# Optimization experiments

Measured on AMD Instinct MI355X. Metric: run time of the kernel, lower is better.

## Reference

```python
import jax, jax.numpy as jnp
import numpy as np

HIDDEN = 2048
NUM_HEADS = 16
HEAD_DIM = 128
INNER = NUM_HEADS * HEAD_DIM
ROPE_BASE = 10000.0


def apply_rope(x):
    # x: [B, H, S, D], rotate-half (NeoX-style) RoPE
    B, H, S, D = x.shape
    inv_freq = 1.0 / (ROPE_BASE ** (jnp.arange(0, D, 2, dtype=jnp.float32) / D))
    t = jnp.arange(S, dtype=jnp.float32)
    freqs = t[:, None] * inv_freq[None, :]          # [S, D/2]
    cos = jnp.concatenate([jnp.cos(freqs)] * 2, -1)  # [S, D]
    sin = jnp.concatenate([jnp.sin(freqs)] * 2, -1)
    x1, x2 = x[..., : D // 2], x[..., D // 2:]
    rotated = jnp.concatenate([-x2, x1], axis=-1)
    return x * cos[None, None] + rotated * sin[None, None]


def setup_inputs() -> dict:
    key = jax.random.key(0)
    ks = jax.random.split(key, 9)
    s = 1.0 / np.sqrt(HIDDEN)
    return {
        "hidden_states": jax.random.normal(ks[0], (2, 2048, HIDDEN), jnp.float32),
        "Wq": jax.random.uniform(ks[1], (INNER, HIDDEN), jnp.float32, -s, s),
        "bq": jax.random.uniform(ks[2], (INNER,), jnp.float32, -s, s),
        "Wk": jax.random.uniform(ks[3], (INNER, HIDDEN), jnp.float32, -s, s),
        "bk": jax.random.uniform(ks[4], (INNER,), jnp.float32, -s, s),
        "Wv": jax.random.uniform(ks[5], (INNER, HIDDEN), jnp.float32, -s, s),
        "bv": jax.random.uniform(ks[6], (INNER,), jnp.float32, -s, s),
        "Wo": jax.random.uniform(ks[7], (HIDDEN, INNER), jnp.float32, -s, s),
        "bo": jax.random.uniform(ks[8], (HIDDEN,), jnp.float32, -s, s),
    }


def reference(hidden_states, Wq, bq, Wk, bk, Wv, bv, Wo, bo):
    B, S, _ = hidden_states.shape

    def heads(x):  # [B,S,inner] -> [B,H,S,D]
        return x.reshape(B, S, NUM_HEADS, HEAD_DIM).transpose(0, 2, 1, 3)

    q = heads(hidden_states @ Wq.T + bq)
    k = heads(hidden_states @ Wk.T + bk)
    v = heads(hidden_states @ Wv.T + bv)
    q = apply_rope(q)
    k = apply_rope(k)

    scores = jnp.einsum("bhqd,bhkd->bhqk", q, k) / jnp.sqrt(
        jnp.asarray(HEAD_DIM, q.dtype))
    causal = jnp.tril(jnp.ones((S, S), dtype=bool))
    scores = jnp.where(causal[None, None], scores, jnp.finfo(scores.dtype).min)
    weights = jax.nn.softmax(scores, axis=-1)
    context = jnp.einsum("bhqk,bhkd->bhqd", weights, v)
    merged = context.transpose(0, 2, 1, 3).reshape(B, S, INNER)
    return merged @ Wo.T + bo
```

## Files before the change

kernel.cpp:

```cpp
#include <hip/hip_runtime.h>

using u16 = unsigned short;
using u32 = unsigned int;

typedef __attribute__((ext_vector_type(4))) float f32x4;
typedef __attribute__((ext_vector_type(8))) short frag8;

#define HIDDEN 2048
#define SEQ    2048
#define NHEADS 16
#define HDIM   128

__device__ __forceinline__ float bf2f(u16 u) {
  union { u32 i; float f; } c; c.i = ((u32)u) << 16; return c.f;
}
__device__ __forceinline__ u16 f2bf(float f) {
  union { float f; u32 i; } c; c.f = f;
  u32 u = c.i + 0x7fffu + ((c.i >> 16) & 1u);
  return (u16)(u >> 16);
}

__global__ void cvt_all(const float* __restrict__ X,
                        const float* __restrict__ W0, const float* __restrict__ W1,
                        const float* __restrict__ W2, const float* __restrict__ W3,
                        u16* __restrict__ dX,
                        u16* __restrict__ dW0, u16* __restrict__ dW1,
                        u16* __restrict__ dW2, u16* __restrict__ dW3)
{
  const int bx = blockIdx.x;
  const float* s; u16* d; int g;
  if (bx < 4096) { s = X; d = dX; g = bx * 256 + threadIdx.x; }
  else {
    const int t = bx - 4096;
    const int w = t >> 11;
    s = (w == 0) ? W0 : (w == 1) ? W1 : (w == 2) ? W2 : W3;
    d = (w == 0) ? dW0 : (w == 1) ? dW1 : (w == 2) ? dW2 : dW3;
    g = (t & 2047) * 256 + threadIdx.x;
  }
  const float* p = s + (size_t)g * 8;
  f32x4 x0 = *(const f32x4*)p, x1 = *(const f32x4*)(p + 4);
  frag8 o;
#pragma unroll
  for (int e = 0; e < 4; e++) { o[e] = (short)f2bf(x0[e]); o[e+4] = (short)f2bf(x1[e]); }
  *(frag8*)(d + (size_t)g * 8) = o;
}

template<int W_BF16, int NW, int VT, int C_F32>
__global__ __launch_bounds__(256, 4)
void gemm_fused(const u16* __restrict__ A,
                const void* __restrict__ W0, const void* __restrict__ W1,
                const void* __restrict__ W2,
                const float* __restrict__ bias0, const float* __restrict__ bias1,
                const float* __restrict__ bias2,
                void* __restrict__ C0, void* __restrict__ C1, void* __restrict__ C2)
{
  __shared__ __align__(16) u16 smem[8192];
  u16* As = smem;
  u16* Bs = smem + 4096;

  const int tid  = threadIdx.x;
  const int lane = tid & 63;
  const int wv   = tid >> 6;
  const int quad = lane >> 4;
  const int l16  = lane & 15;
  const int wm = wv >> 1, wn = wv & 1;
  const int m0 = blockIdx.y * 128;
  const int wix = (NW == 1) ? 0 : (blockIdx.x >> 4);
  const int n0  = ((NW == 1) ? blockIdx.x : (blockIdx.x & 15)) * 128;

  const void* Wp = (wix == 0) ? W0 : (wix == 1) ? W1 : W2;
  const float* bias = (wix == 0) ? bias0 : (wix == 1) ? bias1 : bias2;
  void* Cp = (wix == 0) ? C0 : (wix == 1) ? C1 : C2;

  f32x4 acc[4][4];
#pragma unroll
  for (int i = 0; i < 4; i++)
#pragma unroll
    for (int j = 0; j < 4; j++) acc[i][j] = (f32x4)0.0f;

  const int g0 = tid, g1 = tid + 256;
  const int r0 = g0 >> 2, c0 = (g0 & 3) * 8;
  const int r1 = g1 >> 2, c1 = (g1 & 3) * 8;

  for (int k0 = 0; k0 < HIDDEN; k0 += 32) {
    __builtin_amdgcn_global_load_lds(
      (const __attribute__((address_space(1))) void*)(A + (size_t)(m0 + r0) * HIDDEN + k0 + c0),
      (__attribute__((address_space(3))) void*)(As + g0 * 8), 16, 0, 0);
    __builtin_amdgcn_global_load_lds(
      (const __attribute__((address_space(1))) void*)(A + (size_t)(m0 + r1) * HIDDEN + k0 + c1),
      (__attribute__((address_space(3))) void*)(As + g1 * 8), 16, 0, 0);
    if (W_BF16) {
      const u16* Wb = (const u16*)Wp;
      __builtin_amdgcn_global_load_lds(
        (const __attribute__((address_space(1))) void*)(Wb + (size_t)(n0 + r0) * HIDDEN + k0 + c0),
        (__attribute__((address_space(3))) void*)(Bs + g0 * 8), 16, 0, 0);
      __builtin_amdgcn_global_load_lds(
        (const __attribute__((address_space(1))) void*)(Wb + (size_t)(n0 + r1) * HIDDEN + k0 + c1),
        (__attribute__((address_space(3))) void*)(Bs + g1 * 8), 16, 0, 0);
    } else {
      const float* Wf = (const float*)Wp;
      const float* p0 = Wf + (size_t)(n0 + r0) * HIDDEN + k0 + c0;
      const float* p1 = Wf + (size_t)(n0 + r1) * HIDDEN + k0 + c1;
      f32x4 x0 = *(const f32x4*)p0, x1 = *(const f32x4*)(p0 + 4);
      f32x4 y0 = *(const f32x4*)p1, y1 = *(const f32x4*)(p1 + 4);
      frag8 b0v, b1v;
#pragma unroll
      for (int e = 0; e < 4; e++) {
        b0v[e]   = (short)f2bf(x0[e]); b0v[e+4] = (short)f2bf(x1[e]);
        b1v[e]   = (short)f2bf(y0[e]); b1v[e+4] = (short)f2bf(y1[e]);
      }
      *(frag8*)&Bs[g0 * 8] = b0v;
      *(frag8*)&Bs[g1 * 8] = b1v;
    }

    __builtin_amdgcn_s_waitcnt(0);
    __syncthreads();

    frag8 af[4], bfr[4];
#pragma unroll
    for (int mt = 0; mt < 4; mt++)
      af[mt] = *(const frag8*)&As[(wm*64 + mt*16 + l16) * 32 + quad*8];
#pragma unroll
    for (int nt = 0; nt < 4; nt++)
      bfr[nt] = *(const frag8*)&Bs[(wn*64 + nt*16 + l16) * 32 + quad*8];
#pragma unroll
    for (int mt = 0; mt < 4; mt++)
#pragma unroll
      for (int nt = 0; nt < 4; nt++)
        acc[mt][nt] = __builtin_amdgcn_mfma_f32_16x16x32_bf16(af[mt], bfr[nt], acc[mt][nt], 0, 0, 0);

    __syncthreads();
  }

  if (VT && wix == 2) {
    u16* Cv = (u16*)Cp;
    u16* T = smem + wv * 1056;
#pragma unroll
    for (int nt = 0; nt < 4; nt++) {
      const int n  = n0 + wn*64 + nt*16 + l16;
      const float bv = bias[n];
#pragma unroll
      for (int mt = 0; mt < 4; mt++)
#pragma unroll
        for (int r = 0; r < 4; r++)
          T[l16 * 66 + mt*16 + quad*4 + r] = f2bf(acc[mt][nt][r] + bv);
#pragma unroll
      for (int rr = 0; rr < 16; rr++) {
        const int nn = n0 + wn*64 + nt*16 + rr;
        const int mm = m0 + wm*64 + lane;
        const int b = mm >> 11, s = mm & 2047;
        Cv[((size_t)(b * HIDDEN + nn)) * SEQ + s] = T[rr * 66 + lane];
      }
    }
  } else {
#pragma unroll
    for (int nt = 0; nt < 4; nt++) {
      const int n  = n0 + wn*64 + nt*16 + l16;
      const float bv = bias[n];
#pragma unroll
      for (int mt = 0; mt < 4; mt++) {
#pragma unroll
        for (int r = 0; r < 4; r++) {
          const int m = m0 + wm*64 + mt*16 + quad*4 + r;
          if (C_F32) ((float*)Cp)[(size_t)m * HIDDEN + n] = acc[mt][nt][r] + bv;
          else       ((u16*)Cp)[(size_t)m * HIDDEN + n]   = f2bf(acc[mt][nt][r] + bv);
        }
      }
    }
  }
}

#define NT32 32

#define STG(gptr, lofs) __builtin_amdgcn_global_load_lds( \
    (const __attribute__((address_space(1))) void*)(gptr), \
    (__attribute__((address_space(3))) void*)(smem + (lofs)), 16, 0, 0)

#define GRP(t, DOSTAGE, WAITSTR) { \
  u16* As = smem + ((t) % 3) * 24576; \
  u16* Bs = As + 16384; \
  frag8 af[8], bfr[2]; \
  _Pragma("unroll") for (int mt = 0; mt < 8; mt++) \
    af[mt] = *(const frag8*)(As + abase + mt*1024 + s0q); \
  bfr[0] = *(const frag8*)(Bs + bbase + s0q); \
  bfr[1] = *(const frag8*)(Bs + bbase + 1024 + s0q); \
  if (DOSTAGE) { \
    const size_t ko = (size_t)((t)+2)*64; const int sb = (((t)+2)%3)*24576; \
    STG(gA0 + ko, sb + ldsA0); STG(gA1 + ko, sb + ldsA1); STG(gB0 + ko, sb + ldsB0); \
  } \
  __builtin_amdgcn_s_barrier(); \
  __builtin_amdgcn_s_setprio(1); \
  _Pragma("unroll") for (int mt = 0; mt < 8; mt++) { \
    acc[mt][0] = __builtin_amdgcn_mfma_f32_16x16x32_bf16(af[mt], bfr[0], acc[mt][0], 0,0,0); \
    acc[mt][1] = __builtin_amdgcn_mfma_f32_16x16x32_bf16(af[mt], bfr[1], acc[mt][1], 0,0,0); \
  } \
  __builtin_amdgcn_s_setprio(0); \
  __builtin_amdgcn_s_barrier(); \
  _Pragma("unroll") for (int mt = 0; mt < 8; mt++) \
    af[mt] = *(const frag8*)(As + abase + mt*1024 + s1q); \
  bfr[0] = *(const frag8*)(Bs + bbase + s1q); \
  bfr[1] = *(const frag8*)(Bs + bbase + 1024 + s1q); \
  if (DOSTAGE) { \
    const size_t ko = (size_t)((t)+2)*64; const int sb = (((t)+2)%3)*24576; \
    STG(gA2 + ko, sb + ldsA2); STG(gA3 + ko, sb + ldsA3); STG(gB1 + ko, sb + ldsB1); \
  } \
  __builtin_amdgcn_s_barrier(); \
  __builtin_amdgcn_s_setprio(1); \
  _Pragma("unroll") for (int mt = 0; mt < 8; mt++) { \
    acc[mt][0] = __builtin_amdgcn_mfma_f32_16x16x32_bf16(af[mt], bfr[0], acc[mt][0], 0,0,0); \
    acc[mt][1] = __builtin_amdgcn_mfma_f32_16x16x32_bf16(af[mt], bfr[1], acc[mt][1], 0,0,0); \
  } \
  __builtin_amdgcn_s_setprio(0); \
  asm volatile("s_waitcnt " WAITSTR ::: "memory"); \
  __builtin_amdgcn_s_barrier(); \
}

__global__ __launch_bounds__(512, 2)
void gemm256_qkv(const u16* __restrict__ A,
                 const u16* __restrict__ W0, const u16* __restrict__ W1,
                 const u16* __restrict__ W2,
                 const float* __restrict__ bias0, const float* __restrict__ bias1,
                 const float* __restrict__ bias2,
                 u16* __restrict__ C0, u16* __restrict__ C1, u16* __restrict__ Vt)
{
  __shared__ __align__(16) u16 smem[73728];

  const int tid  = threadIdx.x;
  const int lane = tid & 63;
  const int wv   = tid >> 6;
  const int quad = lane >> 4;
  const int l16  = lane & 15;
  const int wm = wv >> 2, wn = wv & 3;

  const int bid = blockIdx.x;
  const int sbid = (bid & 7) * 96 + (bid >> 3);
  const int colTile = sbid >> 4;
  const int rowTile = sbid & 15;
  const int wix = colTile >> 4;
  const int n0  = (colTile & 15) * 128;
  const int m0  = rowTile * 256;

  const u16* Wp = (wix == 0) ? W0 : (wix == 1) ? W1 : W2;
  const float* bias = (wix == 0) ? bias0 : (wix == 1) ? bias1 : bias2;

  const int c8 = (lane & 7) ^ (lane >> 3);
  const int rA = lane >> 3;
  const u16* gA0 = A  + (size_t)(m0 + wv*32 +  0 + rA) * HIDDEN + c8*8;
  const u16* gA1 = A  + (size_t)(m0 + wv*32 +  8 + rA) * HIDDEN + c8*8;
  const u16* gA2 = A  + (size_t)(m0 + wv*32 + 16 + rA) * HIDDEN + c8*8;
  const u16* gA3 = A  + (size_t)(m0 + wv*32 + 24 + rA) * HIDDEN + c8*8;
  const u16* gB0 = Wp + (size_t)(n0 + wv*16 +  0 + rA) * HIDDEN + c8*8;
  const u16* gB1 = Wp + (size_t)(n0 + wv*16 +  8 + rA) * HIDDEN + c8*8;
  const int ldsA0 = (4*wv)*512 + lane*8;
  const int ldsA1 = ldsA0 + 512;
  const int ldsA2 = ldsA0 + 1024;
  const int ldsA3 = ldsA0 + 1536;
  const int ldsB0 = 16384 + (2*wv)*512 + lane*8;
  const int ldsB1 = ldsB0 + 512;

  const int s0q = ((quad    ) ^ (l16 & 7)) * 8;
  const int s1q = ((quad + 4) ^ (l16 & 7)) * 8;
  const int abase = (wm*128 + l16) * 64;
  const int bbase = (wn*32  + l16) * 64;

  f32x4 acc[8][2];
#pragma unroll
  for (int i = 0; i < 8; i++) { acc[i][0] = (f32x4)0.0f; acc[i][1] = (f32x4)0.0f; }

  STG(gA0, ldsA0); STG(gA1, ldsA1); STG(gB0, ldsB0);
  STG(gA2, ldsA2); STG(gA3, ldsA3); STG(gB1, ldsB1);
  STG(gA0 + 64, 24576 + ldsA0); STG(gA1 + 64, 24576 + ldsA1); STG(gB0 + 64, 24576 + ldsB0);
  STG(gA2 + 64, 24576 + ldsA2); STG(gA3 + 64, 24576 + ldsA3); STG(gB1 + 64, 24576 + ldsB1);
  asm volatile("s_waitcnt vmcnt(6)" ::: "memory");
  __builtin_amdgcn_s_barrier();

  for (int t = 0; t < NT32 - 2; ++t) GRP(t, 1, "vmcnt(6)");
  GRP(NT32 - 2, 0, "vmcnt(0)");
  GRP(NT32 - 1, 0, "vmcnt(63)");

  if (wix != 2) {
    u16* Cb = (wix == 0) ? C0 : C1;
#pragma unroll
    for (int nt = 0; nt < 2; nt++) {
      const int n = n0 + wn*32 + nt*16 + l16;
      const float bv = bias[n];
#pragma unroll
      for (int mt = 0; mt < 8; mt++) {
        const int m = m0 + wm*128 + mt*16 + quad*4;
#pragma unroll
        for (int r = 0; r < 4; r++)
          Cb[(size_t)(m + r) * HIDDEN + n] = f2bf(acc[mt][nt][r] + bv);
      }
    }
  } else {
    u16* T = smem + wv * 2176;
    const int b  = m0 >> 11;
    const int s0 = (m0 & 2047) + wm*128;
#pragma unroll
    for (int nt = 0; nt < 2; nt++) {
      const int nloc = n0 + wn*32 + nt*16;
      const float bv = bias[nloc + l16];
#pragma unroll
      for (int mt = 0; mt < 8; mt++)
#pragma unroll
        for (int r = 0; r < 4; r++)
          T[l16*136 + mt*16 + quad*4 + r] = f2bf(acc[mt][nt][r] + bv);
#pragma unroll
      for (int rr = 0; rr < 16; rr++) {
        const size_t vb = ((size_t)(b * HIDDEN + nloc + rr)) * SEQ + s0;
        Vt[vb + lane]      = T[rr*136 + lane];
        Vt[vb + 64 + lane] = T[rr*136 + 64 + lane];
      }
    }
  }
}

__global__ void rope_kernel(u16* __restrict__ Q, u16* __restrict__ K)
{
  const int tid = blockIdx.x * 256 + threadIdx.x;
  const int t   = tid >> 19;
  const int r   = tid & 524287;
  const int row = r >> 7;
  const int grp = r & 127;
  const int h   = grp >> 3, d0 = (grp & 7) * 8;
  u16* X = t ? K : Q;
  const float s = (float)(row & 2047);
  const float qscale = t ? 1.0f : 0.08838834764831845f;
  const size_t base = (size_t)row * HIDDEN + h * HDIM + d0;
  frag8 a = *(const frag8*)(X + base);
  frag8 b = *(const frag8*)(X + base + 64);
  frag8 oa, ob;
#pragma unroll
  for (int e = 0; e < 8; e++) {
    const float inv = __expf(-(float)(d0 + e) * (9.210340371976184f / 64.0f));
    float sn, c;
    __sincosf(s * inv, &sn, &c);
    const float x1 = bf2f((u16)a[e]), x2 = bf2f((u16)b[e]);
    oa[e] = (short)f2bf((x1 * c - x2 * sn) * qscale);
    ob[e] = (short)f2bf((x2 * c + x1 * sn) * qscale);
  }
  *(frag8*)(X + base)      = oa;
  *(frag8*)(X + base + 64) = ob;
}

#define KS_STR 132
#define VS_STR 68
#define PS_STR 68
__global__ __launch_bounds__(256, 3)
void attn_kernel(const u16* Q, const u16* __restrict__ K,
                 const u16* __restrict__ Vt, u16* O)
{
  __shared__ __align__(16) u16 Ks[64 * KS_STR];
  __shared__ __align__(16) u16 Vs[128 * VS_STR];
  __shared__ __align__(16) u16 Ps[4 * 16 * PS_STR];

  const int bx = blockIdx.x;
  const int g  = bx >> 5;
  const int bh = bx & 31;
  const int qt = (g & 1) ? (31 - (g >> 1)) : (g >> 1);
  const int b = bh >> 4, h = bh & 15;

  const int tid = threadIdx.x, lane = tid & 63, wv = tid >> 6;
  const int quad = lane >> 4, l16 = lane & 15;

  frag8 qf[4];
  const size_t qbase = ((size_t)(b * SEQ) + qt*64 + wv*16) * HIDDEN + h * HDIM;
#pragma unroll
  for (int ks = 0; ks < 4; ks++)
    qf[ks] = *(const frag8*)(Q + qbase + (size_t)l16 * HIDDEN + ks*32 + quad*8);

  f32x4 Oacc[8];
#pragma unroll
  for (int dt = 0; dt < 8; dt++) Oacc[dt] = (f32x4)0.0f;
  float m_i[4], l_i[4];
#pragma unroll
  for (int r = 0; r < 4; r++) { m_i[r] = -1e30f; l_i[r] = 0.0f; }

  const int ktmax = qt + 1;
  const size_t krow0 = (size_t)(b * SEQ) * HIDDEN + h * HDIM;
  const size_t vrow0 = (size_t)(b * HIDDEN + h * HDIM) * SEQ;
  u16* Pw = Ps + wv * (16 * PS_STR);
  const int qmin = qt*64 + wv*16;

  for (int kt = 0; kt < ktmax; kt++) {
#pragma unroll
    for (int it = 0; it < 4; it++) {
      const int G = it * 256 + tid;
      const int key = G >> 4, gd = (G & 15) * 8;
      *(frag8*)&Ks[key * KS_STR + gd] =
        *(const frag8*)(K + krow0 + (size_t)(kt*64 + key) * HIDDEN + gd);
    }
#pragma unroll
    for (int it = 0; it < 4; it++) {
      const int G = it * 256 + tid;
      const int d = G >> 3, j8 = (G & 7) * 8;
      *(frag8*)&Vs[d * VS_STR + j8] =
        *(const frag8*)(Vt + vrow0 + (size_t)d * SEQ + kt*64 + j8);
    }
    __syncthreads();

    f32x4 st[4];
#pragma unroll
    for (int jt = 0; jt < 4; jt++) st[jt] = (f32x4)0.0f;

#pragma unroll
    for (int ks = 0; ks < 4; ks++) {
      frag8 kf[4];
#pragma unroll
      for (int jt = 0; jt < 4; jt++)
        kf[jt] = *(const frag8*)&Ks[(jt*16 + l16) * KS_STR + ks*32 + quad*8];
#pragma unroll
      for (int jt = 0; jt < 4; jt++)
        st[jt] = __builtin_amdgcn_mfma_f32_16x16x32_bf16(qf[ks], kf[jt], st[jt], 0, 0, 0);
    }

    if (kt == qt) {
#pragma unroll
      for (int jt = 0; jt < 4; jt++) {
        const int jl = jt*16 + l16;
#pragma unroll
        for (int r = 0; r < 4; r++) {
          const int ml = wv*16 + quad*4 + r;
          st[jt][r] = (jl <= ml) ? st[jt][r] : -1e30f;
        }
      }
    }

    float alpha[4];
#pragma unroll
    for (int r = 0; r < 4; r++) {
      float cm = st[0][r];
#pragma unroll
      for (int jt = 1; jt < 4; jt++) cm = fmaxf(cm, st[jt][r]);
      cm = fmaxf(cm, __shfl_xor(cm, 1, 64));
      cm = fmaxf(cm, __shfl_xor(cm, 2, 64));
      cm = fmaxf(cm, __shfl_xor(cm, 4, 64));
      cm = fmaxf(cm, __shfl_xor(cm, 8, 64));
      const float mnew = fmaxf(m_i[r], cm);
      alpha[r] = __expf(m_i[r] - mnew);
      m_i[r] = mnew;
    }

    float csum[4];
#pragma unroll
    for (int r = 0; r < 4; r++) csum[r] = 0.0f;
#pragma unroll
    for (int jt = 0; jt < 4; jt++)
#pragma unroll
      for (int r = 0; r < 4; r++) {
        const float p = __expf(st[jt][r] - m_i[r]);
        csum[r] += p;
        Pw[(quad*4 + r) * PS_STR + jt*16 + l16] = f2bf(p);
      }
#pragma unroll
    for (int r = 0; r < 4; r++) {
      float cs = csum[r];
      cs += __shfl_xor(cs, 1, 64);
      cs += __shfl_xor(cs, 2, 64);
      cs += __shfl_xor(cs, 4, 64);
      cs += __shfl_xor(cs, 8, 64);
      l_i[r] = l_i[r] * alpha[r] + cs;
#pragma unroll
      for (int dt = 0; dt < 8; dt++) Oacc[dt][r] *= alpha[r];
    }

#pragma unroll
    for (int ks2 = 0; ks2 < 2; ks2++) {
      frag8 pf = *(const frag8*)&Pw[l16 * PS_STR + ks2*32 + quad*8];
#pragma unroll
      for (int dt = 0; dt < 8; dt++) {
        frag8 vf = *(const frag8*)&Vs[(dt*16 + l16) * VS_STR + ks2*32 + quad*8];
        Oacc[dt] = __builtin_amdgcn_mfma_f32_16x16x32_bf16(pf, vf, Oacc[dt], 0, 0, 0);
      }
    }
    __syncthreads();
  }

#pragma unroll
  for (int r = 0; r < 4; r++) {
    const float inv = 1.0f / l_i[r];
    const int m = qmin + quad*4 + r;
#pragma unroll
    for (int dt = 0; dt < 8; dt++) {
      const int d = dt*16 + l16;
      O[((size_t)(b * SEQ) + m) * HIDDEN + h * HDIM + d] = f2bf(Oacc[dt][r] * inv);
    }
  }
}

extern "C" void kernel_launch(void* const* d_in, const int* in_sizes, int n_in,
                              void* d_out, int out_size, void* d_ws, size_t ws_size,
                              hipStream_t stream)
{
  const float* X  = (const float*)d_in[0];
  const float* Wq = (const float*)d_in[1];
  const float* bq = (const float*)d_in[2];
  const float* Wk = (const float*)d_in[3];
  const float* bk = (const float*)d_in[4];
  const float* Wv = (const float*)d_in[5];
  const float* bv = (const float*)d_in[6];
  const float* Wo = (const float*)d_in[7];
  const float* bo = (const float*)d_in[8];
  float* out = (float*)d_out;

  u16* Kb = (u16*)d_out;
  u16* Xb = (u16*)d_out + (8u << 20);
  char* ws = (char*)d_ws;
  u16* Qb  = (u16*)ws;
  u16* Vtb = (u16*)(ws + (16u << 20));

  dim3 blk(256);
  const bool fast = ws_size >= (64u << 20);
  if (fast) {
    u16* Wqb = (u16*)(ws + (32u << 20));
    u16* Wkb = (u16*)(ws + (40u << 20));
    u16* Wvb = (u16*)(ws + (48u << 20));
    u16* Wob = (u16*)(ws + (56u << 20));
    cvt_all<<<12288, blk, 0, stream>>>(X, Wq, Wk, Wv, Wo, Xb, Wqb, Wkb, Wvb, Wob);
    gemm256_qkv<<<dim3(768), dim3(512), 0, stream>>>(
        Xb, Wqb, Wkb, Wvb, bq, bk, bv, Qb, Kb, Vtb);
    rope_kernel<<<4096, blk, 0, stream>>>(Qb, Kb);
    attn_kernel<<<1024, blk, 0, stream>>>(Qb, Kb, Vtb, Qb);
    gemm_fused<1,1,0,1><<<dim3(16,32), blk, 0, stream>>>(
        Qb, Wob, Wob, Wob, bo, bo, bo, out, out, out);
  } else {
    cvt_all<<<4096, blk, 0, stream>>>(X, Wq, Wk, Wv, Wo, Xb, Xb, Xb, Xb, Xb);
    gemm_fused<0,3,1,0><<<dim3(48,32), blk, 0, stream>>>(
        Xb, Wq, Wk, Wv, bq, bk, bv, Qb, Kb, Vtb);
    rope_kernel<<<4096, blk, 0, stream>>>(Qb, Kb);
    attn_kernel<<<1024, blk, 0, stream>>>(Qb, Kb, Vtb, Qb);
    gemm_fused<0,1,0,1><<<dim3(16,32), blk, 0, stream>>>(
        Qb, Wo, Wo, Wo, bo, bo, bo, out, out, out);
  }
}
```

Before: 428.3 us.

## Use 256-tile GEMM for output projection and prefetch K/V in attention

Factors the 256x128 tiled GEMM mainloop into a shared macro and adds a new output-projection kernel that uses it in place of the generic fused GEMM. The attention kernel now prefetches the next K/V tile into registers while computing the current one, raises wave priority around its MFMA blocks, and skips rescaling the output accumulator unless the running max grows by more than a threshold. These target global-load latency in attention and lower GEMM efficiency in the output projection. The prefetch adds register pressure, and the lazy rescale lets exponents grow up to e^8 before renormalising, which could affect precision.

```diff
diff --git a/kernel.cpp b/kernel.cpp
--- a/kernel.cpp
+++ b/kernel.cpp
@@ -215,6 +215,44 @@
   __builtin_amdgcn_s_barrier(); \
 }
 
+#define G256_SETUP(Abase, Wbase) \
+  const int tid  = threadIdx.x; \
+  const int lane = tid & 63; \
+  const int wv   = tid >> 6; \
+  const int quad = lane >> 4; \
+  const int l16  = lane & 15; \
+  const int wm = wv >> 2, wn = wv & 3; \
+  const int c8 = (lane & 7) ^ (lane >> 3); \
+  const int rA = lane >> 3; \
+  const u16* gA0 = (Abase) + (size_t)(m0 + wv*32 +  0 + rA) * HIDDEN + c8*8; \
+  const u16* gA1 = (Abase) + (size_t)(m0 + wv*32 +  8 + rA) * HIDDEN + c8*8; \
+  const u16* gA2 = (Abase) + (size_t)(m0 + wv*32 + 16 + rA) * HIDDEN + c8*8; \
+  const u16* gA3 = (Abase) + (size_t)(m0 + wv*32 + 24 + rA) * HIDDEN + c8*8; \
+  const u16* gB0 = (Wbase) + (size_t)(n0 + wv*16 +  0 + rA) * HIDDEN + c8*8; \
+  const u16* gB1 = (Wbase) + (size_t)(n0 + wv*16 +  8 + rA) * HIDDEN + c8*8; \
+  const int ldsA0 = (4*wv)*512 + lane*8; \
+  const int ldsA1 = ldsA0 + 512; \
+  const int ldsA2 = ldsA0 + 1024; \
+  const int ldsA3 = ldsA0 + 1536; \
+  const int ldsB0 = 16384 + (2*wv)*512 + lane*8; \
+  const int ldsB1 = ldsB0 + 512; \
+  const int s0q = ((quad    ) ^ (l16 & 7)) * 8; \
+  const int s1q = ((quad + 4) ^ (l16 & 7)) * 8; \
+  const int abase = (wm*128 + l16) * 64; \
+  const int bbase = (wn*32  + l16) * 64; \
+  f32x4 acc[8][2]; \
+  _Pragma("unroll") \
+  for (int i = 0; i < 8; i++) { acc[i][0] = (f32x4)0.0f; acc[i][1] = (f32x4)0.0f; } \
+  STG(gA0, ldsA0); STG(gA1, ldsA1); STG(gB0, ldsB0); \
+  STG(gA2, ldsA2); STG(gA3, ldsA3); STG(gB1, ldsB1); \
+  STG(gA0 + 64, 24576 + ldsA0); STG(gA1 + 64, 24576 + ldsA1); STG(gB0 + 64, 24576 + ldsB0); \
+  STG(gA2 + 64, 24576 + ldsA2); STG(gA3 + 64, 24576 + ldsA3); STG(gB1 + 64, 24576 + ldsB1); \
+  asm volatile("s_waitcnt vmcnt(6)" ::: "memory"); \
+  __builtin_amdgcn_s_barrier(); \
+  for (int t = 0; t < NT32 - 2; ++t) GRP(t, 1, "vmcnt(6)"); \
+  GRP(NT32 - 2, 0, "vmcnt(0)"); \
+  GRP(NT32 - 1, 0, "vmcnt(63)");
+
 __global__ __launch_bounds__(512, 2)
 void gemm256_qkv(const u16* __restrict__ A,
                  const u16* __restrict__ W0, const u16* __restrict__ W1,
@@ -225,13 +263,6 @@
 {
   __shared__ __align__(16) u16 smem[73728];
 
-  const int tid  = threadIdx.x;
-  const int lane = tid & 63;
-  const int wv   = tid >> 6;
-  const int quad = lane >> 4;
-  const int l16  = lane & 15;
-  const int wm = wv >> 2, wn = wv & 3;
-
   const int bid = blockIdx.x;
   const int sbid = (bid & 7) * 96 + (bid >> 3);
   const int colTile = sbid >> 4;
@@ -243,40 +274,7 @@
   const u16* Wp = (wix == 0) ? W0 : (wix == 1) ? W1 : W2;
   const float* bias = (wix == 0) ? bias0 : (wix == 1) ? bias1 : bias2;
 
-  const int c8 = (lane & 7) ^ (lane >> 3);
-  const int rA = lane >> 3;
-  const u16* gA0 = A  + (size_t)(m0 + wv*32 +  0 + rA) * HIDDEN + c8*8;
-  const u16* gA1 = A  + (size_t)(m0 + wv*32 +  8 + rA) * HIDDEN + c8*8;
-  const u16* gA2 = A  + (size_t)(m0 + wv*32 + 16 + rA) * HIDDEN + c8*8;
-  const u16* gA3 = A  + (size_t)(m0 + wv*32 + 24 + rA) * HIDDEN + c8*8;
-  const u16* gB0 = Wp + (size_t)(n0 + wv*16 +  0 + rA) * HIDDEN + c8*8;
-  const u16* gB1 = Wp + (size_t)(n0 + wv*16 +  8 + rA) * HIDDEN + c8*8;
-  const int ldsA0 = (4*wv)*512 + lane*8;
-  const int ldsA1 = ldsA0 + 512;
-  const int ldsA2 = ldsA0 + 1024;
-  const int ldsA3 = ldsA0 + 1536;
-  const int ldsB0 = 16384 + (2*wv)*512 + lane*8;
-  const int ldsB1 = ldsB0 + 512;
-
-  const int s0q = ((quad    ) ^ (l16 & 7)) * 8;
-  const int s1q = ((quad + 4) ^ (l16 & 7)) * 8;
-  const int abase = (wm*128 + l16) * 64;
-  const int bbase = (wn*32  + l16) * 64;
-
-  f32x4 acc[8][2];
-#pragma unroll
-  for (int i = 0; i < 8; i++) { acc[i][0] = (f32x4)0.0f; acc[i][1] = (f32x4)0.0f; }
-
-  STG(gA0, ldsA0); STG(gA1, ldsA1); STG(gB0, ldsB0);
-  STG(gA2, ldsA2); STG(gA3, ldsA3); STG(gB1, ldsB1);
-  STG(gA0 + 64, 24576 + ldsA0); STG(gA1 + 64, 24576 + ldsA1); STG(gB0 + 64, 24576 + ldsB0);
-  STG(gA2 + 64, 24576 + ldsA2); STG(gA3 + 64, 24576 + ldsA3); STG(gB1 + 64, 24576 + ldsB1);
-  asm volatile("s_waitcnt vmcnt(6)" ::: "memory");
-  __builtin_amdgcn_s_barrier();
-
-  for (int t = 0; t < NT32 - 2; ++t) GRP(t, 1, "vmcnt(6)");
-  GRP(NT32 - 2, 0, "vmcnt(0)");
-  GRP(NT32 - 1, 0, "vmcnt(63)");
+  G256_SETUP(A, Wp)
 
   if (wix != 2) {
     u16* Cb = (wix == 0) ? C0 : C1;
@@ -311,6 +309,35 @@
         Vt[vb + lane]      = T[rr*136 + lane];
         Vt[vb + 64 + lane] = T[rr*136 + 64 + lane];
       }
+    }
+  }
+}
+
+__global__ __launch_bounds__(512, 2)
+void gemm256_o(const u16* __restrict__ A, const u16* __restrict__ W,
+               const float* __restrict__ bias, float* __restrict__ C)
+{
+  __shared__ __align__(16) u16 smem[73728];
+
+  const int bid = blockIdx.x;
+  const int sbid = (bid & 7) * 32 + (bid >> 3);
+  const int colTile = sbid >> 4;
+  const int rowTile = sbid & 15;
+  const int n0  = colTile * 128;
+  const int m0  = rowTile * 256;
+
+  G256_SETUP(A, W)
+
+#pragma unroll
+  for (int nt = 0; nt < 2; nt++) {
+    const int n = n0 + wn*32 + nt*16 + l16;
+    const float bv = bias[n];
+#pragma unroll
+    for (int mt = 0; mt < 8; mt++) {
+      const int m = m0 + wm*128 + mt*16 + quad*4;
+#pragma unroll
+      for (int r = 0; r < 4; r++)
+        C[(size_t)(m + r) * HIDDEN + n] = acc[mt][nt][r] + bv;
     }
   }
 }
@@ -382,27 +409,37 @@
   u16* Pw = Ps + wv * (16 * PS_STR);
   const int qmin = qt*64 + wv*16;
 
+  const int kkey = tid >> 4, kgd = (tid & 15) * 8;
+  const int vd = tid >> 3, vj8 = (tid & 7) * 8;
+
+  frag8 kreg[4], vreg[4];
+#pragma unroll
+  for (int it = 0; it < 4; it++) {
+    kreg[it] = *(const frag8*)(K + krow0 + (size_t)(it*16 + kkey) * HIDDEN + kgd);
+    vreg[it] = *(const frag8*)(Vt + vrow0 + (size_t)(it*32 + vd) * SEQ + vj8);
+  }
+
   for (int kt = 0; kt < ktmax; kt++) {
 #pragma unroll
     for (int it = 0; it < 4; it++) {
-      const int G = it * 256 + tid;
-      const int key = G >> 4, gd = (G & 15) * 8;
-      *(frag8*)&Ks[key * KS_STR + gd] =
-        *(const frag8*)(K + krow0 + (size_t)(kt*64 + key) * HIDDEN + gd);
-    }
-#pragma unroll
-    for (int it = 0; it < 4; it++) {
-      const int G = it * 256 + tid;
-      const int d = G >> 3, j8 = (G & 7) * 8;
-      *(frag8*)&Vs[d * VS_STR + j8] =
-        *(const frag8*)(Vt + vrow0 + (size_t)d * SEQ + kt*64 + j8);
+      *(frag8*)&Ks[(it*16 + kkey) * KS_STR + kgd] = kreg[it];
+      *(frag8*)&Vs[(it*32 + vd) * VS_STR + vj8]  = vreg[it];
     }
     __syncthreads();
 
+    if (kt + 1 < ktmax) {
+#pragma unroll
+      for (int it = 0; it < 4; it++) {
+        kreg[it] = *(const frag8*)(K + krow0 + (size_t)((kt+1)*64 + it*16 + kkey) * HIDDEN + kgd);
+        vreg[it] = *(const frag8*)(Vt + vrow0 + (size_t)(it*32 + vd) * SEQ + (kt+1)*64 + vj8);
+      }
+    }
+
     f32x4 st[4];
 #pragma unroll
     for (int jt = 0; jt < 4; jt++) st[jt] = (f32x4)0.0f;
 
+    __builtin_amdgcn_s_setprio(1);
 #pragma unroll
     for (int ks = 0; ks < 4; ks++) {
       frag8 kf[4];
@@ -413,6 +450,7 @@
       for (int jt = 0; jt < 4; jt++)
         st[jt] = __builtin_amdgcn_mfma_f32_16x16x32_bf16(qf[ks], kf[jt], st[jt], 0, 0, 0);
     }
+    __builtin_amdgcn_s_setprio(0);
 
     if (kt == qt) {
 #pragma unroll
@@ -427,6 +465,7 @@
     }
 
     float alpha[4];
+    int needresc = 0;
 #pragma unroll
     for (int r = 0; r < 4; r++) {
       float cm = st[0][r];
@@ -436,9 +475,13 @@
       cm = fmaxf(cm, __shfl_xor(cm, 2, 64));
       cm = fmaxf(cm, __shfl_xor(cm, 4, 64));
       cm = fmaxf(cm, __shfl_xor(cm, 8, 64));
-      const float mnew = fmaxf(m_i[r], cm);
-      alpha[r] = __expf(m_i[r] - mnew);
-      m_i[r] = mnew;
+      if (cm > m_i[r] + 8.0f) {
+        alpha[r] = __expf(m_i[r] - cm);
+        m_i[r] = cm;
+        needresc = 1;
+      } else {
+        alpha[r] = 1.0f;
+      }
     }
 
     float csum[4];
@@ -460,10 +503,15 @@
       cs += __shfl_xor(cs, 4, 64);
       cs += __shfl_xor(cs, 8, 64);
       l_i[r] = l_i[r] * alpha[r] + cs;
-#pragma unroll
-      for (int dt = 0; dt < 8; dt++) Oacc[dt][r] *= alpha[r];
-    }
-
+    }
+    if (__any(needresc)) {
+#pragma unroll
+      for (int r = 0; r < 4; r++)
+#pragma unroll
+        for (int dt = 0; dt < 8; dt++) Oacc[dt][r] *= alpha[r];
+    }
+
+    __builtin_amdgcn_s_setprio(1);
 #pragma unroll
     for (int ks2 = 0; ks2 < 2; ks2++) {
       frag8 pf = *(const frag8*)&Pw[l16 * PS_STR + ks2*32 + quad*8];
@@ -473,6 +521,7 @@
         Oacc[dt] = __builtin_amdgcn_mfma_f32_16x16x32_bf16(pf, vf, Oacc[dt], 0, 0, 0);
       }
     }
+    __builtin_amdgcn_s_setprio(0);
     __syncthreads();
   }
 
@@ -521,8 +570,7 @@
         Xb, Wqb, Wkb, Wvb, bq, bk, bv, Qb, Kb, Vtb);
     rope_kernel<<<4096, blk, 0, stream>>>(Qb, Kb);
     attn_kernel<<<1024, blk, 0, stream>>>(Qb, Kb, Vtb, Qb);
-    gemm_fused<1,1,0,1><<<dim3(16,32), blk, 0, stream>>>(
-        Qb, Wob, Wob, Wob, bo, bo, bo, out, out, out);
+    gemm256_o<<<dim3(256), dim3(512), 0, stream>>>(Qb, Wob, bo, out);
   } else {
     cvt_all<<<4096, blk, 0, stream>>>(X, Wq, Wk, Wv, Wo, Xb, Xb, Xb, Xb, Xb);
     gemm_fused<0,3,1,0><<<dim3(48,32), blk, 0, stream>>>(
```

After: 429.5 us. About the same (+0.3%).
